# Kernel tuning notes

Measured on AMD Instinct MI355X. Metric: run time of the kernel, lower is better.

## Reference

```python
import jax, jax.numpy as jnp
import numpy as np


def _transition_matrix(durations, max_seq_len):
    # durations: (B, L_enc) int; returns (B, L_enc, L_dec) float32
    rng = jnp.arange(max_seq_len)                         # (L_dec,)
    cs = jnp.cumsum(durations, axis=1)[..., None]         # (B, L_enc, 1)
    mask1 = rng < cs
    # torch .roll(1) without dim flattens -> roll -> reshape; jnp.roll(axis=None) matches
    shifted = jnp.roll(durations, 1)
    shifted = shifted.at[:, 0].set(0)
    cs2 = jnp.cumsum(shifted, axis=1)[..., None]
    mask2 = rng < cs2
    tm = mask1 & (~mask2)
    return tm.astype(jnp.float32)


def setup_inputs() -> dict:
    key = jax.random.key(0)
    k1, k2 = jax.random.split(key)
    B, L_enc, E = 32, 512, 256
    L_dec = 2048
    encoder_output = jax.random.normal(k1, (B, L_enc, E), dtype=jnp.float32)
    durations = jax.random.randint(k2, (B, L_enc), 0, 8, dtype=jnp.int64)
    return {
        "encoder_output": encoder_output,
        "durations": durations,
        "decoder_max_seq_len": L_dec,
    }


def reference(encoder_output, durations, decoder_max_seq_len):
    tm = _transition_matrix(durations, decoder_max_seq_len)   # (B, L_enc, L_dec)
    # bmm(enc^T, tm)^T  ==  einsum over L_enc
    return jnp.einsum("ble,bld->bde", encoder_output, tm)     # (B, L_dec, E)
```

## Files before the change

### kernel.cpp

```cpp
#include <hip/hip_runtime.h>

#define B_    32
#define LENC  512
#define LDEC  2048
#define E_    256
#define E4    (E_ / 4)

__global__ __launch_bounds__(LENC) void build_idx_kernel(
    const int* __restrict__ dur, int* __restrict__ idx) {
  const int b = blockIdx.x;
  const int t = threadIdx.x;

  __shared__ int s[LENC];
  const int v = dur[b * LENC + t];

#pragma unroll
  for (int i = 0; i < LDEC / LENC; ++i)
    idx[b * LDEC + i * LENC + t] = -1;

  s[t] = v;
  __syncthreads();

#pragma unroll
  for (int off = 1; off < LENC; off <<= 1) {
    const int add = (t >= off) ? s[t - off] : 0;
    __syncthreads();
    s[t] += add;
    __syncthreads();
  }

  const int incl = s[t];
  const int excl = incl - v;
  const int start = min(excl, LDEC);
  const int end   = min(incl, LDEC);
  for (int d = start; d < end; ++d)
    idx[b * LDEC + d] = t;
}

__global__ __launch_bounds__(256) void gather_rows_kernel(
    const float4* __restrict__ enc, const int* __restrict__ idx,
    float4* __restrict__ out) {
  const int row  = (blockIdx.x * blockDim.x + threadIdx.x) >> 6;
  const int lane = threadIdx.x & 63;
  const int b = row >> 11;
  const int l = idx[row];

  float4 val = make_float4(0.f, 0.f, 0.f, 0.f);
  if (l >= 0)
    val = enc[(size_t)(b * LENC + l) * E4 + lane];
  out[(size_t)row * E4 + lane] = val;
}

extern "C" void kernel_launch(void* const* d_in, const int* in_sizes, int n_in,
                              void* d_out, int out_size, void* d_ws, size_t ws_size,
                              hipStream_t stream) {
  const float* enc = (const float*)d_in[0];
  const int*   dur = (const int*)d_in[1];

  int* idx = (int*)d_ws;

  build_idx_kernel<<<B_, LENC, 0, stream>>>(dur, idx);

  const int rows = B_ * LDEC;
  const int threads = rows * 64;
  gather_rows_kernel<<<threads / 256, 256, 0, stream>>>(
      (const float4*)enc, idx, (float4*)d_out);
}
```

Measured before the change: 91.31 us.

## Fuse index build into gather with per-block scan and binary search

Replaces the two-kernel pipeline (scan-and-scatter index build, then row gather) with one fused kernel. Each block recomputes the batch's cumulative durations using a wave-shuffle scan, binary-searches the source row for its decoder rows, and then copies encoder rows directly to the output. This removes a launch, the workspace index array round trip, and the serial single-block-per-batch index kernel. In exchange every block redundantly reloads and rescans the 512 durations, and each wave now handles 8 rows sequentially.

New measurement: 88.09 us. 3.5% less time.

```diff
diff --git a/kernel.cpp b/kernel.cpp
--- a/kernel.cpp
+++ b/kernel.cpp
@@ -3,52 +3,59 @@
 #define B_    32
 #define LENC  512
 #define LDEC  2048
-#define E_    256
-#define E4    (E_ / 4)
+#define E4    64
+#define TPB   256
+#define NWAVE (TPB / 64)
+#define ROWS_PER_BLOCK 32
+#define ROWS_PER_WAVE  (ROWS_PER_BLOCK / NWAVE)
 
-__global__ __launch_bounds__(LENC) void build_idx_kernel(
-    const int* __restrict__ dur, int* __restrict__ idx) {
-  const int b = blockIdx.x;
-  const int t = threadIdx.x;
+__global__ __launch_bounds__(TPB) void length_regulator_fused(
+    const float4* __restrict__ enc, const int2* __restrict__ dur2,
+    float4* __restrict__ out) {
+  const int t    = threadIdx.x;
+  const int lane = t & 63;
+  const int wid  = t >> 6;
+  const int b    = blockIdx.y;
 
-  __shared__ int s[LENC];
-  const int v = dur[b * LENC + t];
+  __shared__ int cs[LENC];
+  __shared__ int wsum[NWAVE];
 
+  const int2 v = dur2[b * (LENC / 2) + t];
+  int x = v.x + v.y;
 #pragma unroll
-  for (int i = 0; i < LDEC / LENC; ++i)
-    idx[b * LDEC + i * LENC + t] = -1;
-
-  s[t] = v;
+  for (int off = 1; off < 64; off <<= 1) {
+    const int y = __shfl_up(x, off, 64);
+    if (lane >= off) x += y;
+  }
+  if (lane == 63) wsum[wid] = x;
+  __syncthreads();
+  int wo = 0;
+#pragma unroll
+  for (int w = 0; w < NWAVE; ++w) wo += (w < wid) ? wsum[w] : 0;
+  const int ip = x + wo;
+  cs[2 * t + 1] = ip;
+  cs[2 * t]     = ip - v.y;
   __syncthreads();
 
-#pragma unroll
-  for (int off = 1; off < LENC; off <<= 1) {
-    const int add = (t >= off) ? s[t - off] : 0;
-    __syncthreads();
-    s[t] += add;
-    __syncthreads();
+  const int total = cs[LENC - 1];
+  int d = blockIdx.x * ROWS_PER_BLOCK + wid * ROWS_PER_WAVE;
+
+  int lo = 0, hi = LENC;
+  while (lo < hi) {
+    const int mid = (lo + hi) >> 1;
+    if (cs[mid] <= d) lo = mid + 1; else hi = mid;
   }
 
-  const int incl = s[t];
-  const int excl = incl - v;
-  const int start = min(excl, LDEC);
-  const int end   = min(incl, LDEC);
-  for (int d = start; d < end; ++d)
-    idx[b * LDEC + d] = t;
-}
-
-__global__ __launch_bounds__(256) void gather_rows_kernel(
-    const float4* __restrict__ enc, const int* __restrict__ idx,
-    float4* __restrict__ out) {
-  const int row  = (blockIdx.x * blockDim.x + threadIdx.x) >> 6;
-  const int lane = threadIdx.x & 63;
-  const int b = row >> 11;
-  const int l = idx[row];
-
-  float4 val = make_float4(0.f, 0.f, 0.f, 0.f);
-  if (l >= 0)
-    val = enc[(size_t)(b * LENC + l) * E4 + lane];
-  out[(size_t)row * E4 + lane] = val;
+  const size_t enc_base = (size_t)b * LENC * E4;
+  const size_t out_base = (size_t)b * LDEC * E4;
+#pragma unroll
+  for (int r = 0; r < ROWS_PER_WAVE; ++r, ++d) {
+    while (lo < LENC && cs[lo] <= d) ++lo;
+    float4 val = make_float4(0.f, 0.f, 0.f, 0.f);
+    if (d < total)
+      val = enc[enc_base + (size_t)lo * E4 + lane];
+    out[out_base + (size_t)d * E4 + lane] = val;
+  }
 }
 
 extern "C" void kernel_launch(void* const* d_in, const int* in_sizes, int n_in,
@@ -57,12 +64,7 @@
   const float* enc = (const float*)d_in[0];
   const int*   dur = (const int*)d_in[1];
 
-  int* idx = (int*)d_ws;
-
-  build_idx_kernel<<<B_, LENC, 0, stream>>>(dur, idx);
-
-  const int rows = B_ * LDEC;
-  const int threads = rows * 64;
-  gather_rows_kernel<<<threads / 256, 256, 0, stream>>>(
-      (const float4*)enc, idx, (float4*)d_out);
+  dim3 grid(LDEC / ROWS_PER_BLOCK, B_);
+  length_regulator_fused<<<grid, TPB, 0, stream>>>(
+      (const float4*)enc, (const int2*)dur, (float4*)d_out);
 }
```
